# Kernel optimization log

Measured on AMD Instinct MI355X. Metric: run time of the kernel, lower is better.

## Reference

```python
import jax, jax.numpy as jnp
import numpy as np

B, T, D, C = 128, 256, 1280, 100


def setup_inputs() -> dict:
    key = jax.random.key(0)
    ks = jax.random.split(key, 6)
    s = 1.0 / np.sqrt(D)  # PyTorch GRU init scale
    return {
        "seq": jax.random.normal(ks[0], (B, T, D), dtype=jnp.float32),
        "candidates": jax.random.normal(ks[1], (B, C, D), dtype=jnp.float32),
        "W_ih": jax.random.normal(ks[2], (3 * D, D), dtype=jnp.float32) * s,
        "W_hh": jax.random.normal(ks[3], (3 * D, D), dtype=jnp.float32) * s,
        "b_ih": jax.random.normal(ks[4], (3 * D,), dtype=jnp.float32) * s,
        "b_hh": jax.random.normal(ks[5], (3 * D,), dtype=jnp.float32) * s,
    }


def _gru_final_hidden(seq, W_ih, W_hh, b_ih, b_hh):
    # seq: [B, T, D]. PyTorch gate order: r, z, n.
    H = W_hh.shape[1]
    # Precompute input projections for all timesteps: [T, B, 3H]
    x_proj = jnp.einsum('btd,gd->tbg', seq, W_ih) + b_ih
    h0 = jnp.zeros((seq.shape[0], H), dtype=seq.dtype)

    def step(h, xp):
        gi_r, gi_z, gi_n = jnp.split(xp, 3, axis=-1)
        gh = h @ W_hh.T + b_hh  # [B, 3H]
        gh_r, gh_z, gh_n = jnp.split(gh, 3, axis=-1)
        r = jax.nn.sigmoid(gi_r + gh_r)
        z = jax.nn.sigmoid(gi_z + gh_z)
        n = jnp.tanh(gi_n + r * gh_n)
        h_new = (1.0 - z) * n + z * h
        return h_new, None

    h_last, _ = jax.lax.scan(step, h0, x_proj)
    return h_last  # [B, H]


def reference(seq, candidates, W_ih, W_hh, b_ih, b_hh):
    hidden = _gru_final_hidden(seq, W_ih, W_hh, b_ih, b_hh)  # [B, D]
    # einsum '...bd,bcd->...bc' with hidden [1,B,D] then squeeze(0) -> [B, C]
    scores = jnp.einsum('bd,bcd->bc', hidden, candidates)
    return scores
```

## Files before the change

kernel.cpp:

```cpp
#include <hip/hip_runtime.h>
#include <hip/hip_bf16.h>

typedef _Float16 f16;
typedef _Float16 f16x8 __attribute__((ext_vector_type(8)));
typedef float f32x4 __attribute__((ext_vector_type(4)));

#define B_ 128
#define T_ 256
#define D_ 1280
#define G3_ 3840
#define C_ 100
#define TB_ 32768
#define NBUF 16

#define O_H16  0ull
#define O_SEQB 0ull
#define O_WIH  83886080ull
#define O_WHH  93716480ull
#define O_XP   103546880ull
#define O_H32  355860480ull
#define O_BAR  356515840ull

__global__ void k_convert(const float* __restrict__ seq, const float* __restrict__ wih,
                          const float* __restrict__ whh, f16* __restrict__ seqb,
                          f16* __restrict__ wih16, f16* __restrict__ whh16,
                          unsigned* __restrict__ bar) {
  if (blockIdx.x == 0) {
    for (int j = threadIdx.x; j < 10240; j += 256)
      __hip_atomic_store(bar + j, 0u, __ATOMIC_RELAXED, __HIP_MEMORY_SCOPE_AGENT);
  }
  const long NSEQ = (long)TB_ * (D_ / 8);
  const long NW = (long)G3_ * (D_ / 8);
  const long total = NSEQ + 2 * NW;
  for (long i = (long)blockIdx.x * blockDim.x + threadIdx.x; i < total;
       i += (long)gridDim.x * blockDim.x) {
    const float* src;
    f16* dst;
    if (i < NSEQ) {
      long row = i / (D_ / 8), c = i % (D_ / 8);
      long t = row >> 7, b = row & 127;
      src = seq + ((b * T_ + t) * (long)D_ + c * 8);
      dst = seqb + (row * (long)D_ + c * 8);
    } else if (i < NSEQ + NW) {
      long j = i - NSEQ;
      src = wih + j * 8;
      dst = wih16 + j * 8;
    } else {
      long j = i - NSEQ - NW;
      src = whh + j * 8;
      dst = whh16 + j * 8;
    }
    float4 a = *(const float4*)src, b4 = *(const float4*)(src + 4);
    f16x8 o;
    o[0] = (f16)a.x; o[1] = (f16)a.y; o[2] = (f16)a.z; o[3] = (f16)a.w;
    o[4] = (f16)b4.x; o[5] = (f16)b4.y; o[6] = (f16)b4.z; o[7] = (f16)b4.w;
    *(f16x8*)dst = o;
  }
}

__device__ __forceinline__ void gl_lds16(const f16* g, f16* lds) {
  __builtin_amdgcn_global_load_lds((const __attribute__((address_space(1))) void*)g,
                                   (__attribute__((address_space(3))) void*)lds, 16, 0, 0);
}

__global__ __launch_bounds__(256) void k_xproj(const f16* __restrict__ A, const f16* __restrict__ Bw,
                                               const float* __restrict__ bih, f16* __restrict__ Cout) {
  __shared__ f16 Alds[128 * 32];
  __shared__ f16 Blds[128 * 32];
  int bid = blockIdx.x;
  int sb = bid / 240;
  int wi = bid % 240;
  int bm = sb * 8 + (wi & 7);
  int bn = wi >> 3;
  long brow = (long)bm * 128;
  int bcol = bn * 128;
  int tid = threadIdx.x, w = tid >> 6, l = tid & 63;
  int wm = w & 1, wn = w >> 1;

  f32x4 acc[4][4] = {};

  int sr = w * 32 + (l >> 2);
  int sc = (l & 3) * 8;
  const f16* gA = A + (brow + sr) * (long)D_ + sc;
  const f16* gB = Bw + (long)(bcol + sr) * D_ + sc;
  f16* lAw = Alds + (w * 32) * 32;
  f16* lBw = Blds + (w * 32) * 32;

  int fr = l & 15, fc = (l >> 4) * 8;

  for (int kb = 0; kb < 40; ++kb) {
    const f16* a0 = gA + kb * 32;
    const f16* b0 = gB + kb * 32;
    gl_lds16(a0, lAw);
    gl_lds16(a0 + 16 * D_, lAw + 16 * 32);
    gl_lds16(b0, lBw);
    gl_lds16(b0 + 16 * D_, lBw + 16 * 32);
    __syncthreads();
    f16x8 af[4], bf[4];
#pragma unroll
    for (int mt = 0; mt < 4; ++mt) af[mt] = *(const f16x8*)(Alds + (wm * 64 + mt * 16 + fr) * 32 + fc);
#pragma unroll
    for (int nt = 0; nt < 4; ++nt) bf[nt] = *(const f16x8*)(Blds + (wn * 64 + nt * 16 + fr) * 32 + fc);
#pragma unroll
    for (int mt = 0; mt < 4; ++mt)
#pragma unroll
      for (int nt = 0; nt < 4; ++nt)
        acc[mt][nt] = __builtin_amdgcn_mfma_f32_16x16x32_f16(af[mt], bf[nt], acc[mt][nt], 0, 0, 0);
    __syncthreads();
  }
#pragma unroll
  for (int nt = 0; nt < 4; ++nt) {
    int col = bcol + wn * 64 + nt * 16 + fr;
    int g = col / D_;
    int dcol = col - g * D_;
    int cg = dcol >> 4, c16 = dcol & 15;
    float bv = bih[col];
    f16* base = Cout + (((long)bm * 80 + cg) * 3 + g) * 2048 + c16;
#pragma unroll
    for (int mt = 0; mt < 4; ++mt) {
#pragma unroll
      for (int i = 0; i < 4; ++i) {
        int b = wm * 64 + mt * 16 + (l >> 4) * 4 + i;
        base[b * 16] = (f16)(acc[mt][nt][i] + bv);
      }
    }
  }
}

__global__ __launch_bounds__(256, 3) void k_scan(const f16* __restrict__ whh16,
                                                 const f16* __restrict__ xproj,
                                                 const float* __restrict__ bhh,
                                                 f16* __restrict__ h16, float* __restrict__ h32,
                                                 unsigned* __restrict__ bar) {
  __shared__ float red[4][3][256];
  int wg = blockIdx.x;
  int rg = wg & 7, cg = wg >> 3;
  int r0 = rg * 16, d0 = cg * 16;
  int tid = threadIdx.x, w = tid >> 6, l = tid & 63;
  int fr = l & 15, fq = l >> 4;
  int erow = tid >> 4, ecol = tid & 15;
  unsigned* mycnt = bar + (rg * 40 + (cg % 40)) * 32;

  const f16* wbase = whh16 + (long)(d0 + fr) * D_ + w * 320 + fq * 8;
  f16x8 wf[10][3];
#pragma unroll
  for (int j = 0; j < 10; ++j)
#pragma unroll
    for (int g = 0; g < 3; ++g)
      wf[j][g] = *(const f16x8*)(wbase + (long)g * (D_ * D_) + j * 32);

  if ((tid & 1) == 0) {
    unsigned* p = (unsigned*)(h16 + (r0 + erow) * D_ + d0 + ecol);
    __hip_atomic_store(p, 0u, __ATOMIC_RELAXED, __HIP_MEMORY_SCOPE_AGENT);
  }

  float bh0 = bhh[0 * D_ + d0 + ecol];
  float bh1 = bhh[1 * D_ + d0 + ecol];
  float bh2 = bhh[2 * D_ + d0 + ecol];
  float hreg = 0.f;
  f16 xr, xz, xn;

  auto prefetch_x = [&](int tt) {
    const f16* xs = xproj + (((long)tt * 80 + cg) * 3) * 2048 + (r0 + erow) * 16 + ecol;
    xr = xs[0];
    xz = xs[2048];
    xn = xs[4096];
  };
  auto poll = [&](unsigned target) {
    unsigned it = 0;
    for (;;) {
      unsigned v = target;
      if (l < 40)
        v = __hip_atomic_load(bar + (rg * 40 + l) * 32, __ATOMIC_RELAXED, __HIP_MEMORY_SCOPE_AGENT);
      if (__all(v >= target)) break;
      __builtin_amdgcn_s_sleep(1);
      if (++it > 500000u) {
        if (l < 40)
          v = __hip_atomic_fetch_add(bar + (rg * 40 + l) * 32, 0u, __ATOMIC_RELAXED,
                                     __HIP_MEMORY_SCOPE_AGENT);
        if (__all(v >= target)) break;
        it = 0;
      }
    }
  };

  prefetch_x(0);

  __syncthreads();
  if (tid == 0)
    __hip_atomic_fetch_add(mycnt, 1u, __ATOMIC_RELAXED, __HIP_MEMORY_SCOPE_AGENT);
  if (tid < 64) {
    poll(2u);
    if (tid == 0) __builtin_amdgcn_fence(__ATOMIC_ACQUIRE, "agent");
  }
  __syncthreads();

  const f16* abase = (const f16*)h16 + (long)(r0 + fr) * D_ + w * 320 + fq * 8;
  unsigned tgt = 4u;
  for (int t = 0; t < T_; ++t) {
    const f16* arow = abase + (long)(t & (NBUF - 1)) * (B_ * D_);
    f32x4 acc0 = {}, acc1 = {}, acc2 = {};
#pragma unroll
    for (int j = 0; j < 10; ++j) {
      f16x8 a = *(const f16x8*)(arow + j * 32);
      acc0 = __builtin_amdgcn_mfma_f32_16x16x32_f16(a, wf[j][0], acc0, 0, 0, 0);
      acc1 = __builtin_amdgcn_mfma_f32_16x16x32_f16(a, wf[j][1], acc1, 0, 0, 0);
      acc2 = __builtin_amdgcn_mfma_f32_16x16x32_f16(a, wf[j][2], acc2, 0, 0, 0);
    }
#pragma unroll
    for (int i = 0; i < 4; ++i) {
      int pos = (((fq * 4 + i) * 16) + fr) ^ (fq << 2);
      red[w][0][pos] = acc0[i];
      red[w][1][pos] = acc1[i];
      red[w][2][pos] = acc2[i];
    }
    __syncthreads();
    int pr = tid ^ ((tid >> 6) << 2);
    float s0 = red[0][0][pr] + red[1][0][pr] + red[2][0][pr] + red[3][0][pr];
    float s1 = red[0][1][pr] + red[1][1][pr] + red[2][1][pr] + red[3][1][pr];
    float s2 = red[0][2][pr] + red[1][2][pr] + red[2][2][pr] + red[3][2][pr];
    float r = 1.f / (1.f + __expf(-((float)xr + s0 + bh0)));
    float z = 1.f / (1.f + __expf(-((float)xz + s1 + bh1)));
    float pn = (float)xn + r * (s2 + bh2);
    pn = fminf(fmaxf(pn, -30.f), 30.f);
    float e2 = __expf(-2.f * pn);
    float nn = (1.f - e2) / (1.f + e2);
    float hv = (1.f - z) * nn + z * hreg;
    hreg = hv;
    if (t == T_ - 1) break;
    unsigned short bits = __builtin_bit_cast(unsigned short, (f16)hv);
    unsigned other = (unsigned)__shfl_xor((int)bits, 1);
    if ((tid & 1) == 0) {
      unsigned val = (unsigned)bits | (other << 16);
      f16* hn = h16 + (long)((t + 1) & (NBUF - 1)) * (B_ * D_);
      __hip_atomic_store((unsigned*)(hn + (r0 + erow) * D_ + d0 + ecol), val, __ATOMIC_RELAXED,
                         __HIP_MEMORY_SCOPE_AGENT);
    }
    __syncthreads();
    if (tid == 0)
      __hip_atomic_fetch_add(mycnt, 1u, __ATOMIC_RELAXED, __HIP_MEMORY_SCOPE_AGENT);
    prefetch_x(t + 1);
    if (tid < 64) {
      poll(tgt);
      if (tid == 0 && (((t + 1) & (NBUF - 1)) == 0))
        __builtin_amdgcn_fence(__ATOMIC_ACQUIRE, "agent");
    }
    __syncthreads();
    tgt += 2u;
  }
  h32[(r0 + erow) * D_ + d0 + ecol] = hreg;
}

__global__ __launch_bounds__(256) void k_scores(const float* __restrict__ h32,
                                                const float* __restrict__ cand,
                                                float* __restrict__ out) {
  int gw = blockIdx.x * 4 + (threadIdx.x >> 6);
  int l = threadIdx.x & 63;
  int b = gw / C_, c = gw % C_;
  const float* hp = h32 + (long)b * D_;
  const float* cp = cand + ((long)b * C_ + c) * D_;
  float s = 0.f;
#pragma unroll
  for (int q = 0; q < 5; ++q) {
    int d = q * 256 + l * 4;
    float4 hv = *(const float4*)(hp + d);
    float4 cv = *(const float4*)(cp + d);
    s += hv.x * cv.x + hv.y * cv.y + hv.z * cv.z + hv.w * cv.w;
  }
#pragma unroll
  for (int off = 32; off > 0; off >>= 1) s += __shfl_down(s, off);
  if (l == 0) out[(long)b * C_ + c] = s;
}

extern "C" void kernel_launch(void* const* d_in, const int* in_sizes, int n_in, void* d_out,
                              int out_size, void* d_ws, size_t ws_size, hipStream_t stream) {
  const float* seq = (const float*)d_in[0];
  const float* cand = (const float*)d_in[1];
  const float* wih = (const float*)d_in[2];
  const float* whh = (const float*)d_in[3];
  const float* bih = (const float*)d_in[4];
  const float* bhh = (const float*)d_in[5];
  char* ws = (char*)d_ws;
  f16* seqb = (f16*)(ws + O_SEQB);
  f16* wih16 = (f16*)(ws + O_WIH);
  f16* whh16 = (f16*)(ws + O_WHH);
  f16* xp = (f16*)(ws + O_XP);
  f16* h16 = (f16*)(ws + O_H16);
  float* h32 = (float*)(ws + O_H32);
  unsigned* bar = (unsigned*)(ws + O_BAR);

  k_convert<<<2048, 256, 0, stream>>>(seq, wih, whh, seqb, wih16, whh16, bar);
  k_xproj<<<7680, 256, 0, stream>>>(seqb, wih16, bih, xp);
  k_scan<<<640, 256, 0, stream>>>(whh16, xp, bhh, h16, h32, bar);
  k_scores<<<3200, 256, 0, stream>>>(h32, cand, (float*)d_out);
}
```

Baseline: 2.396 ms.

## Process two batch tiles per scan workgroup to reuse W_hh fragments and halve the grid

Each persistent scan workgroup now covers 32 batch rows (two 16-row MFMA tiles) instead of 16. It reuses the register-resident W_hh fragments for both tiles, and the grid shrinks from 640 to 320 workgroups with launch bounds lowered to 2 per CU. An empty asm constraint pins the weight fragments in VGPRs. This cuts duplicated weight loads and the number of workgroups taking part in each per-step barrier. In exchange, each workgroup does twice the MFMA, reduction and gate work per timestep on the serial critical path.

Result: faster. 2.262 ms (-5.6%).

```diff
diff --git a/kernel.cpp b/kernel.cpp
--- a/kernel.cpp
+++ b/kernel.cpp
@@ -127,18 +127,18 @@
   }
 }
 
-__global__ __launch_bounds__(256, 3) void k_scan(const f16* __restrict__ whh16,
+__global__ __launch_bounds__(256, 2) void k_scan(const f16* __restrict__ whh16,
                                                  const f16* __restrict__ xproj,
                                                  const float* __restrict__ bhh,
                                                  f16* __restrict__ h16, float* __restrict__ h32,
                                                  unsigned* __restrict__ bar) {
-  __shared__ float red[4][3][256];
+  __shared__ float red[4][3][2][256];
   int wg = blockIdx.x;
-  int rg = wg & 7, cg = wg >> 3;
-  int r0 = rg * 16, d0 = cg * 16;
+  int rg = wg & 3, cg = wg >> 2;
+  int r0 = rg * 32, d0 = cg * 16;
   int tid = threadIdx.x, w = tid >> 6, l = tid & 63;
   int fr = l & 15, fq = l >> 4;
-  int erow = tid >> 4, ecol = tid & 15;
+  int er = tid >> 4, ec = tid & 15;
   unsigned* mycnt = bar + (rg * 40 + (cg % 40)) * 32;
 
   const f16* wbase = whh16 + (long)(d0 + fr) * D_ + w * 320 + fq * 8;
@@ -148,23 +148,35 @@
 #pragma unroll
     for (int g = 0; g < 3; ++g)
       wf[j][g] = *(const f16x8*)(wbase + (long)g * (D_ * D_) + j * 32);
+#pragma unroll
+  for (int j = 0; j < 10; ++j)
+#pragma unroll
+    for (int g = 0; g < 3; ++g)
+      asm volatile("" : "+v"(wf[j][g]));
 
   if ((tid & 1) == 0) {
-    unsigned* p = (unsigned*)(h16 + (r0 + erow) * D_ + d0 + ecol);
-    __hip_atomic_store(p, 0u, __ATOMIC_RELAXED, __HIP_MEMORY_SCOPE_AGENT);
-  }
-
-  float bh0 = bhh[0 * D_ + d0 + ecol];
-  float bh1 = bhh[1 * D_ + d0 + ecol];
-  float bh2 = bhh[2 * D_ + d0 + ecol];
-  float hreg = 0.f;
-  f16 xr, xz, xn;
+#pragma unroll
+    for (int m = 0; m < 2; ++m) {
+      unsigned* p = (unsigned*)(h16 + (r0 + m * 16 + er) * D_ + d0 + ec);
+      __hip_atomic_store(p, 0u, __ATOMIC_RELAXED, __HIP_MEMORY_SCOPE_AGENT);
+    }
+  }
+
+  float bh0 = bhh[0 * D_ + d0 + ec];
+  float bh1 = bhh[1 * D_ + d0 + ec];
+  float bh2 = bhh[2 * D_ + d0 + ec];
+  float hreg[2] = {0.f, 0.f};
+  f16 xg[2][3];
 
   auto prefetch_x = [&](int tt) {
-    const f16* xs = xproj + (((long)tt * 80 + cg) * 3) * 2048 + (r0 + erow) * 16 + ecol;
-    xr = xs[0];
-    xz = xs[2048];
-    xn = xs[4096];
+    const f16* xs = xproj + (((long)tt * 80 + cg) * 3) * 2048;
+#pragma unroll
+    for (int m = 0; m < 2; ++m) {
+      int off = (r0 + m * 16) * 16 + tid;
+      xg[m][0] = xs[off];
+      xg[m][1] = xs[2048 + off];
+      xg[m][2] = xs[4096 + off];
+    }
   };
   auto poll = [&](unsigned target) {
     unsigned it = 0;
@@ -195,46 +207,57 @@
   }
   __syncthreads();
 
-  const f16* abase = (const f16*)h16 + (long)(r0 + fr) * D_ + w * 320 + fq * 8;
   unsigned tgt = 4u;
   for (int t = 0; t < T_; ++t) {
-    const f16* arow = abase + (long)(t & (NBUF - 1)) * (B_ * D_);
-    f32x4 acc0 = {}, acc1 = {}, acc2 = {};
+    const f16* hc = h16 + (long)(t & (NBUF - 1)) * (B_ * D_);
+    const f16* ar0 = hc + (long)(r0 + fr) * D_ + w * 320 + fq * 8;
+    f32x4 acc[2][3] = {};
 #pragma unroll
     for (int j = 0; j < 10; ++j) {
-      f16x8 a = *(const f16x8*)(arow + j * 32);
-      acc0 = __builtin_amdgcn_mfma_f32_16x16x32_f16(a, wf[j][0], acc0, 0, 0, 0);
-      acc1 = __builtin_amdgcn_mfma_f32_16x16x32_f16(a, wf[j][1], acc1, 0, 0, 0);
-      acc2 = __builtin_amdgcn_mfma_f32_16x16x32_f16(a, wf[j][2], acc2, 0, 0, 0);
-    }
-#pragma unroll
-    for (int i = 0; i < 4; ++i) {
-      int pos = (((fq * 4 + i) * 16) + fr) ^ (fq << 2);
-      red[w][0][pos] = acc0[i];
-      red[w][1][pos] = acc1[i];
-      red[w][2][pos] = acc2[i];
-    }
+      f16x8 a0 = *(const f16x8*)(ar0 + j * 32);
+      f16x8 a1 = *(const f16x8*)(ar0 + 16 * D_ + j * 32);
+      acc[0][0] = __builtin_amdgcn_mfma_f32_16x16x32_f16(a0, wf[j][0], acc[0][0], 0, 0, 0);
+      acc[0][1] = __builtin_amdgcn_mfma_f32_16x16x32_f16(a0, wf[j][1], acc[0][1], 0, 0, 0);
+      acc[0][2] = __builtin_amdgcn_mfma_f32_16x16x32_f16(a0, wf[j][2], acc[0][2], 0, 0, 0);
+      acc[1][0] = __builtin_amdgcn_mfma_f32_16x16x32_f16(a1, wf[j][0], acc[1][0], 0, 0, 0);
+      acc[1][1] = __builtin_amdgcn_mfma_f32_16x16x32_f16(a1, wf[j][1], acc[1][1], 0, 0, 0);
+      acc[1][2] = __builtin_amdgcn_mfma_f32_16x16x32_f16(a1, wf[j][2], acc[1][2], 0, 0, 0);
+    }
+#pragma unroll
+    for (int m = 0; m < 2; ++m)
+#pragma unroll
+      for (int g = 0; g < 3; ++g)
+#pragma unroll
+        for (int i = 0; i < 4; ++i)
+          red[w][g][m][(((fq * 4 + i) * 16) + fr) ^ (fq << 2)] = acc[m][g][i];
     __syncthreads();
     int pr = tid ^ ((tid >> 6) << 2);
-    float s0 = red[0][0][pr] + red[1][0][pr] + red[2][0][pr] + red[3][0][pr];
-    float s1 = red[0][1][pr] + red[1][1][pr] + red[2][1][pr] + red[3][1][pr];
-    float s2 = red[0][2][pr] + red[1][2][pr] + red[2][2][pr] + red[3][2][pr];
-    float r = 1.f / (1.f + __expf(-((float)xr + s0 + bh0)));
-    float z = 1.f / (1.f + __expf(-((float)xz + s1 + bh1)));
-    float pn = (float)xn + r * (s2 + bh2);
-    pn = fminf(fmaxf(pn, -30.f), 30.f);
-    float e2 = __expf(-2.f * pn);
-    float nn = (1.f - e2) / (1.f + e2);
-    float hv = (1.f - z) * nn + z * hreg;
-    hreg = hv;
+    float hnew[2];
+#pragma unroll
+    for (int m = 0; m < 2; ++m) {
+      float s0 = red[0][0][m][pr] + red[1][0][m][pr] + red[2][0][m][pr] + red[3][0][m][pr];
+      float s1 = red[0][1][m][pr] + red[1][1][m][pr] + red[2][1][m][pr] + red[3][1][m][pr];
+      float s2 = red[0][2][m][pr] + red[1][2][m][pr] + red[2][2][m][pr] + red[3][2][m][pr];
+      float r = 1.f / (1.f + __expf(-((float)xg[m][0] + s0 + bh0)));
+      float z = 1.f / (1.f + __expf(-((float)xg[m][1] + s1 + bh1)));
+      float pn = (float)xg[m][2] + r * (s2 + bh2);
+      pn = fminf(fmaxf(pn, -30.f), 30.f);
+      float e2 = __expf(-2.f * pn);
+      float nn = (1.f - e2) / (1.f + e2);
+      hnew[m] = (1.f - z) * nn + z * hreg[m];
+      hreg[m] = hnew[m];
+    }
     if (t == T_ - 1) break;
-    unsigned short bits = __builtin_bit_cast(unsigned short, (f16)hv);
-    unsigned other = (unsigned)__shfl_xor((int)bits, 1);
-    if ((tid & 1) == 0) {
-      unsigned val = (unsigned)bits | (other << 16);
-      f16* hn = h16 + (long)((t + 1) & (NBUF - 1)) * (B_ * D_);
-      __hip_atomic_store((unsigned*)(hn + (r0 + erow) * D_ + d0 + ecol), val, __ATOMIC_RELAXED,
-                         __HIP_MEMORY_SCOPE_AGENT);
+    f16* hn = h16 + (long)((t + 1) & (NBUF - 1)) * (B_ * D_);
+#pragma unroll
+    for (int m = 0; m < 2; ++m) {
+      unsigned short bits = __builtin_bit_cast(unsigned short, (f16)hnew[m]);
+      unsigned other = (unsigned)__shfl_xor((int)bits, 1);
+      if ((tid & 1) == 0) {
+        unsigned val = (unsigned)bits | (other << 16);
+        __hip_atomic_store((unsigned*)(hn + (r0 + m * 16 + er) * D_ + d0 + ec), val,
+                           __ATOMIC_RELAXED, __HIP_MEMORY_SCOPE_AGENT);
+      }
     }
     __syncthreads();
     if (tid == 0)
@@ -248,7 +271,8 @@
     __syncthreads();
     tgt += 2u;
   }
-  h32[(r0 + erow) * D_ + d0 + ecol] = hreg;
+#pragma unroll
+  for (int m = 0; m < 2; ++m) h32[(r0 + m * 16 + er) * D_ + d0 + ec] = hreg[m];
 }
 
 __global__ __launch_bounds__(256) void k_scores(const float* __restrict__ h32,
@@ -291,6 +315,6 @@
 
   k_convert<<<2048, 256, 0, stream>>>(seq, wih, whh, seqb, wih16, whh16, bar);
   k_xproj<<<7680, 256, 0, stream>>>(seqb, wih16, bih, xp);
-  k_scan<<<640, 256, 0, stream>>>(whh16, xp, bhh, h16, h32, bar);
+  k_scan<<<320, 256, 0, stream>>>(whh16, xp, bhh, h16, h32, bar);
   k_scores<<<3200, 256, 0, stream>>>(h32, cand, (float*)d_out);
 }
```
